# Performance work log

Hardware: AMD Instinct MI355X
Metric: run time of the kernel (lower is better)

Reference implementation:

```python
import jax, jax.numpy as jnp
import numpy as np

B, T, ENC, DEC, ATTN = 64, 2048, 512, 512, 256


def setup_inputs() -> dict:
    key = jax.random.key(0)
    k1, k2, k3, k4, k5, k6 = jax.random.split(key, 6)
    enc_out = jax.random.normal(k1, (B, T, ENC), dtype=jnp.float32)
    dec_hidden = jax.random.normal(k2, (B, DEC), dtype=jnp.float32)
    mask = jax.random.randint(k3, (B, T), 0, 2) == 1  # True = masked out
    # learned params (Linear with bias=False); torch Linear weight is [out,in],
    # we store transposed [in,out] for x @ W convention
    s_enc = 1.0 / np.sqrt(ENC)
    s_dec = 1.0 / np.sqrt(DEC)
    s_v = 1.0 / np.sqrt(ATTN)
    W_enc = jax.random.uniform(k4, (ENC, ATTN), jnp.float32, -s_enc, s_enc)
    W_dec = jax.random.uniform(k5, (DEC, ATTN), jnp.float32, -s_dec, s_dec)
    v = jax.random.uniform(k6, (ATTN,), jnp.float32, -s_v, s_v)
    return {"enc_out": enc_out, "dec_hidden": dec_hidden, "mask": mask,
            "W_enc": W_enc, "W_dec": W_dec, "v": v}


def reference(enc_out, dec_hidden, mask, W_enc, W_dec, v):
    # proj_enc: [B,T,A]; proj_dec: [B,1,A]
    proj_enc = jnp.einsum('bte,ea->bta', enc_out, W_enc)
    proj_dec = jnp.einsum('bd,da->ba', dec_hidden, W_dec)[:, None, :]
    # energy: [B,T] -- additive (Bahdanau) score
    energy = jnp.einsum('bta,a->bt', jnp.tanh(proj_enc + proj_dec), v)
    energy = jnp.where(mask, -jnp.inf, energy)
    attn_w = jax.nn.softmax(energy, axis=-1)
    attn_w = jnp.nan_to_num(attn_w, nan=0.0)  # fully-masked rows -> 0
    context = jnp.einsum('bt,bte->be', attn_w, enc_out)
    return context, attn_w
```

## Files before the change

### kernel.cpp

```cpp
#include <hip/hip_runtime.h>
#include <stdint.h>

#define Bx 64
#define Tx 2048
#define ENCx 512
#define ATTx 256

typedef float f4 __attribute__((ext_vector_type(4)));
typedef float f32x4 __attribute__((ext_vector_type(4)));
typedef short bf16x8 __attribute__((ext_vector_type(8)));

__device__ __forceinline__ unsigned short f2bf(float f) {
  union { float f; uint32_t u; } c; c.f = f;
  uint32_t u = c.u;
  u += 0x7fffu + ((u >> 16) & 1u);
  return (unsigned short)(u >> 16);
}

__device__ __forceinline__ uint32_t pk_bf(float lo, float hi) {
  uint32_t a = __float_as_uint(lo) + 0x8000u;
  uint32_t b = __float_as_uint(hi) + 0x8000u;
  return __builtin_amdgcn_perm(b, a, 0x07060302u);
}

__device__ __forceinline__ float ftanh(float x) {
  x = fminf(8.f, fmaxf(-8.f, x));
  float z = __expf(2.f * x);
  return 1.f - __fdividef(2.f, z + 1.f);
}

__global__ void k0_wt(const float* __restrict__ W, unsigned short* __restrict__ WTc) {
  int tid = blockIdx.x * 256 + threadIdx.x;
  int kc = tid >> 13;
  int r = tid & 8191;
  int n = r >> 5;
  int kk = r & 31;
  WTc[tid] = f2bf(W[(kc * 32 + kk) * ATTx + n]);
}

__global__ void k1_pd(const float* __restrict__ dec, const float* __restrict__ Wd,
                      float* __restrict__ pd) {
  __shared__ float ld[512];
  int b = blockIdx.x, a = threadIdx.x;
  ld[a] = dec[b * 512 + a];
  ld[a + 256] = dec[b * 512 + a + 256];
  __syncthreads();
  float s = 0.f;
#pragma unroll 8
  for (int d = 0; d < 512; ++d) s = fmaf(ld[d], Wd[d * ATTx + a], s);
  pd[b * ATTx + a] = s;
}

__global__ __launch_bounds__(256) void k2_energy(
    const float* __restrict__ enc, const unsigned short* __restrict__ WTc,
    const float* __restrict__ pd, const float* __restrict__ v,
    const int* __restrict__ mask, float* __restrict__ energy) {
  __shared__ float pdv[256];
  __shared__ float vvs[256];
  const int tid = threadIdx.x;
  const int wid = tid >> 6;
  const int lane = tid & 63;
  const int q = lane >> 4;
  const int c15 = lane & 15;
  const int m0 = blockIdx.x * 128;
  const int b = m0 >> 11;

  pdv[tid] = pd[b * ATTx + tid];
  vvs[tid] = v[tid];
  __syncthreads();

  const int mrow = m0 + wid * 32 + c15;
  const float* a0p = enc + (size_t)mrow * ENCx + q * 8;
  const float* a1p = a0p + 16 * ENCx;
  const unsigned short* wb = WTc + c15 * 32 + q * 8;

  f32x4 acc[2][16];
#pragma unroll
  for (int mt = 0; mt < 2; ++mt)
#pragma unroll
    for (int ct = 0; ct < 16; ++ct) { f32x4 z = {0.f,0.f,0.f,0.f}; acc[mt][ct] = z; }

  for (int kc = 0; kc < 16; ++kc) {
    f4 x0 = *(const f4*)(a0p + kc * 32);
    f4 x1 = *(const f4*)(a0p + kc * 32 + 4);
    f4 y0 = *(const f4*)(a1p + kc * 32);
    f4 y1 = *(const f4*)(a1p + kc * 32 + 4);
    bf16x8 bfr[16];
    const unsigned short* wkc = wb + kc * 8192;
#pragma unroll
    for (int ct = 0; ct < 16; ++ct)
      bfr[ct] = *(const bf16x8*)(wkc + ct * 512);

    union { uint32_t u[4]; bf16x8 v; } am0, am1;
    am0.u[0] = pk_bf(x0.x, x0.y); am0.u[1] = pk_bf(x0.z, x0.w);
    am0.u[2] = pk_bf(x1.x, x1.y); am0.u[3] = pk_bf(x1.z, x1.w);
    am1.u[0] = pk_bf(y0.x, y0.y); am1.u[1] = pk_bf(y0.z, y0.w);
    am1.u[2] = pk_bf(y1.x, y1.y); am1.u[3] = pk_bf(y1.z, y1.w);

#pragma unroll
    for (int ct = 0; ct < 16; ++ct) {
      acc[0][ct] = __builtin_amdgcn_mfma_f32_16x16x32_bf16(am0.v, bfr[ct], acc[0][ct], 0, 0, 0);
      acc[1][ct] = __builtin_amdgcn_mfma_f32_16x16x32_bf16(am1.v, bfr[ct], acc[1][ct], 0, 0, 0);
    }
  }

  float ps[2][4];
#pragma unroll
  for (int mt = 0; mt < 2; ++mt)
#pragma unroll
    for (int i = 0; i < 4; ++i) ps[mt][i] = 0.f;
#pragma unroll
  for (int ct = 0; ct < 16; ++ct) {
    float pv = pdv[ct * 16 + c15];
    float vv = vvs[ct * 16 + c15];
#pragma unroll
    for (int mt = 0; mt < 2; ++mt)
#pragma unroll
      for (int i = 0; i < 4; ++i)
        ps[mt][i] += ftanh(acc[mt][ct][i] + pv) * vv;
  }
#pragma unroll
  for (int s = 1; s < 16; s <<= 1)
#pragma unroll
    for (int mt = 0; mt < 2; ++mt)
#pragma unroll
      for (int i = 0; i < 4; ++i)
        ps[mt][i] += __shfl_xor(ps[mt][i], s, 64);
  if (c15 == 0) {
#pragma unroll
    for (int mt = 0; mt < 2; ++mt)
#pragma unroll
      for (int i = 0; i < 4; ++i) {
        int gm = m0 + wid * 32 + mt * 16 + q * 4 + i;
        energy[gm] = mask[gm] ? -1e30f : ps[mt][i];
      }
  }
}

__global__ void k3_softmax(const float* __restrict__ energy, float* __restrict__ attn) {
  __shared__ float redm[4];
  __shared__ float redl[4];
  int b = blockIdx.x, tid = threadIdx.x;
  int lane = tid & 63, wid = tid >> 6;
  float e[8];
#pragma unroll
  for (int i = 0; i < 8; ++i) e[i] = energy[b * Tx + tid + i * 256];
  float m = e[0];
#pragma unroll
  for (int i = 1; i < 8; ++i) m = fmaxf(m, e[i]);
#pragma unroll
  for (int s = 1; s < 64; s <<= 1) m = fmaxf(m, __shfl_xor(m, s, 64));
  if (lane == 0) redm[wid] = m;
  __syncthreads();
  m = fmaxf(fmaxf(redm[0], redm[1]), fmaxf(redm[2], redm[3]));
  bool dead = (m < -1e29f);
  float w[8];
  float l = 0.f;
#pragma unroll
  for (int i = 0; i < 8; ++i) { w[i] = dead ? 0.f : __expf(e[i] - m); l += w[i]; }
#pragma unroll
  for (int s = 1; s < 64; s <<= 1) l += __shfl_xor(l, s, 64);
  if (lane == 0) redl[wid] = l;
  __syncthreads();
  l = redl[0] + redl[1] + redl[2] + redl[3];
  float inv = dead ? 0.f : __fdividef(1.f, l);
#pragma unroll
  for (int i = 0; i < 8; ++i) attn[b * Tx + tid + i * 256] = w[i] * inv;
}

__global__ void k4_ctx(const float* __restrict__ enc, const float* __restrict__ attn,
                       float* __restrict__ part) {
  __shared__ float wl[128];
  __shared__ f4 comb[128];
  int tc = blockIdx.x & 15, b = blockIdx.x >> 4;
  int tid = threadIdx.x;
  if (tid < 128) wl[tid] = attn[b * Tx + tc * 128 + tid];
  __syncthreads();
  int tl = tid >> 7;
  int ef = tid & 127;
  f4 a = {0.f, 0.f, 0.f, 0.f};
  const f4* base = (const f4*)(enc + ((size_t)b * Tx + tc * 128) * ENCx) + ef;
  for (int t = tl; t < 128; t += 2) {
    f4 x = base[(size_t)t * 128];
    a += x * wl[t];
  }
  if (tl == 1) comb[ef] = a;
  __syncthreads();
  if (tl == 0) {
    a += comb[ef];
    *((f4*)(part + ((size_t)tc * 64 + b) * 512) + ef) = a;
  }
}

__global__ void k5_red(const float* __restrict__ part, float* __restrict__ ctx) {
  int idx = blockIdx.x * 256 + threadIdx.x;
  float s = 0.f;
#pragma unroll
  for (int tc = 0; tc < 16; ++tc) s += part[tc * 32768 + idx];
  ctx[idx] = s;
}

extern "C" void kernel_launch(void* const* d_in, const int* in_sizes, int n_in,
                              void* d_out, int out_size, void* d_ws, size_t ws_size,
                              hipStream_t stream) {
  const float* enc   = (const float*)d_in[0];
  const float* dec   = (const float*)d_in[1];
  const int*   mask  = (const int*)d_in[2];
  const float* W_enc = (const float*)d_in[3];
  const float* W_dec = (const float*)d_in[4];
  const float* v     = (const float*)d_in[5];
  float* ctx  = (float*)d_out;
  float* attn = ctx + Bx * ENCx;
  char* ws = (char*)d_ws;
  unsigned short* WTc = (unsigned short*)ws;
  float* pd     = (float*)(ws + 262144);
  float* energy = (float*)(ws + 262144 + 65536);
  float* part   = (float*)(ws + 262144 + 65536 + 524288);

  k0_wt<<<512, 256, 0, stream>>>(W_enc, WTc);
  k1_pd<<<64, 256, 0, stream>>>(dec, W_dec, pd);
  k2_energy<<<1024, 256, 0, stream>>>(enc, WTc, pd, v, mask, energy);
  k3_softmax<<<64, 256, 0, stream>>>(energy, attn);
  k4_ctx<<<1024, 256, 0, stream>>>(enc, attn, part);
  k5_red<<<128, 256, 0, stream>>>(part, ctx);
}
```

Baseline: 488.0 us.

## Split energy GEMM columns across waves and double the context grid

```diff
diff --git a/kernel.cpp b/kernel.cpp
--- a/kernel.cpp
+++ b/kernel.cpp
@@ -51,89 +51,105 @@
   pd[b * ATTx + a] = s;
 }
 
-__global__ __launch_bounds__(256) void k2_energy(
+__global__ __launch_bounds__(256, 4) void k2_energy(
     const float* __restrict__ enc, const unsigned short* __restrict__ WTc,
     const float* __restrict__ pd, const float* __restrict__ v,
     const int* __restrict__ mask, float* __restrict__ energy) {
   __shared__ float pdv[256];
   __shared__ float vvs[256];
+  __shared__ float ep[4][32];
   const int tid = threadIdx.x;
   const int wid = tid >> 6;
   const int lane = tid & 63;
   const int q = lane >> 4;
   const int c15 = lane & 15;
-  const int m0 = blockIdx.x * 128;
+  const int m0 = blockIdx.x * 32;
   const int b = m0 >> 11;
 
   pdv[tid] = pd[b * ATTx + tid];
   vvs[tid] = v[tid];
   __syncthreads();
 
-  const int mrow = m0 + wid * 32 + c15;
-  const float* a0p = enc + (size_t)mrow * ENCx + q * 8;
-  const float* a1p = a0p + 16 * ENCx;
-  const unsigned short* wb = WTc + c15 * 32 + q * 8;
-
-  f32x4 acc[2][16];
-#pragma unroll
-  for (int mt = 0; mt < 2; ++mt)
-#pragma unroll
-    for (int ct = 0; ct < 16; ++ct) { f32x4 z = {0.f,0.f,0.f,0.f}; acc[mt][ct] = z; }
-
+  const float* a0 = enc + (size_t)(m0 + c15) * ENCx + q * 8;
+  const float* a1 = a0 + 16 * ENCx;
+  const unsigned short* wb = WTc + (wid * 64 + c15) * 32 + q * 8;
+
+  f32x4 acc[2][4];
+#pragma unroll
+  for (int rt = 0; rt < 2; ++rt)
+#pragma unroll
+    for (int ct = 0; ct < 4; ++ct) { f32x4 z = {0.f,0.f,0.f,0.f}; acc[rt][ct] = z; }
+
+  f4 cur0a = *(const f4*)(a0);
+  f4 cur0b = *(const f4*)(a0 + 4);
+  f4 cur1a = *(const f4*)(a1);
+  f4 cur1b = *(const f4*)(a1 + 4);
+
+#pragma unroll 4
   for (int kc = 0; kc < 16; ++kc) {
-    f4 x0 = *(const f4*)(a0p + kc * 32);
-    f4 x1 = *(const f4*)(a0p + kc * 32 + 4);
-    f4 y0 = *(const f4*)(a1p + kc * 32);
-    f4 y1 = *(const f4*)(a1p + kc * 32 + 4);
-    bf16x8 bfr[16];
+    f4 nxt0a, nxt0b, nxt1a, nxt1b;
+    if (kc < 15) {
+      const float* p0 = a0 + (kc + 1) * 32;
+      const float* p1 = a1 + (kc + 1) * 32;
+      nxt0a = *(const f4*)(p0);
+      nxt0b = *(const f4*)(p0 + 4);
+      nxt1a = *(const f4*)(p1);
+      nxt1b = *(const f4*)(p1 + 4);
+    }
+    bf16x8 bfr[4];
     const unsigned short* wkc = wb + kc * 8192;
 #pragma unroll
-    for (int ct = 0; ct < 16; ++ct)
+    for (int ct = 0; ct < 4; ++ct)
       bfr[ct] = *(const bf16x8*)(wkc + ct * 512);
 
     union { uint32_t u[4]; bf16x8 v; } am0, am1;
-    am0.u[0] = pk_bf(x0.x, x0.y); am0.u[1] = pk_bf(x0.z, x0.w);
-    am0.u[2] = pk_bf(x1.x, x1.y); am0.u[3] = pk_bf(x1.z, x1.w);
-    am1.u[0] = pk_bf(y0.x, y0.y); am1.u[1] = pk_bf(y0.z, y0.w);
-    am1.u[2] = pk_bf(y1.x, y1.y); am1.u[3] = pk_bf(y1.z, y1.w);
-
-#pragma unroll
-    for (int ct = 0; ct < 16; ++ct) {
+    am0.u[0] = pk_bf(cur0a.x, cur0a.y); am0.u[1] = pk_bf(cur0a.z, cur0a.w);
+    am0.u[2] = pk_bf(cur0b.x, cur0b.y); am0.u[3] = pk_bf(cur0b.z, cur0b.w);
+    am1.u[0] = pk_bf(cur1a.x, cur1a.y); am1.u[1] = pk_bf(cur1a.z, cur1a.w);
+    am1.u[2] = pk_bf(cur1b.x, cur1b.y); am1.u[3] = pk_bf(cur1b.z, cur1b.w);
+
+#pragma unroll
+    for (int ct = 0; ct < 4; ++ct) {
       acc[0][ct] = __builtin_amdgcn_mfma_f32_16x16x32_bf16(am0.v, bfr[ct], acc[0][ct], 0, 0, 0);
       acc[1][ct] = __builtin_amdgcn_mfma_f32_16x16x32_bf16(am1.v, bfr[ct], acc[1][ct], 0, 0, 0);
     }
+    cur0a = nxt0a; cur0b = nxt0b; cur1a = nxt1a; cur1b = nxt1b;
   }
 
   float ps[2][4];
 #pragma unroll
-  for (int mt = 0; mt < 2; ++mt)
-#pragma unroll
-    for (int i = 0; i < 4; ++i) ps[mt][i] = 0.f;
-#pragma unroll
-  for (int ct = 0; ct < 16; ++ct) {
-    float pv = pdv[ct * 16 + c15];
-    float vv = vvs[ct * 16 + c15];
-#pragma unroll
-    for (int mt = 0; mt < 2; ++mt)
+  for (int rt = 0; rt < 2; ++rt)
+#pragma unroll
+    for (int i = 0; i < 4; ++i) ps[rt][i] = 0.f;
+#pragma unroll
+  for (int ct = 0; ct < 4; ++ct) {
+    int col = wid * 64 + ct * 16 + c15;
+    float pv = pdv[col];
+    float vv = vvs[col];
+#pragma unroll
+    for (int rt = 0; rt < 2; ++rt)
 #pragma unroll
       for (int i = 0; i < 4; ++i)
-        ps[mt][i] += ftanh(acc[mt][ct][i] + pv) * vv;
+        ps[rt][i] += ftanh(acc[rt][ct][i] + pv) * vv;
   }
 #pragma unroll
   for (int s = 1; s < 16; s <<= 1)
 #pragma unroll
-    for (int mt = 0; mt < 2; ++mt)
+    for (int rt = 0; rt < 2; ++rt)
 #pragma unroll
       for (int i = 0; i < 4; ++i)
-        ps[mt][i] += __shfl_xor(ps[mt][i], s, 64);
-  if (c15 == 0) {
-#pragma unroll
-    for (int mt = 0; mt < 2; ++mt)
-#pragma unroll
-      for (int i = 0; i < 4; ++i) {
-        int gm = m0 + wid * 32 + mt * 16 + q * 4 + i;
-        energy[gm] = mask[gm] ? -1e30f : ps[mt][i];
-      }
+        ps[rt][i] += __shfl_xor(ps[rt][i], s, 64);
+  if (c15 == 0)
+#pragma unroll
+    for (int rt = 0; rt < 2; ++rt)
+#pragma unroll
+      for (int i = 0; i < 4; ++i)
+        ep[wid][rt * 16 + q * 4 + i] = ps[rt][i];
+  __syncthreads();
+  if (tid < 32) {
+    float e = ep[0][tid] + ep[1][tid] + ep[2][tid] + ep[3][tid];
+    int gm = m0 + tid;
+    energy[gm] = mask[gm] ? -1e30f : e;
   }
 }
 
@@ -168,25 +184,30 @@
   for (int i = 0; i < 8; ++i) attn[b * Tx + tid + i * 256] = w[i] * inv;
 }
 
-__global__ void k4_ctx(const float* __restrict__ enc, const float* __restrict__ attn,
-                       float* __restrict__ part) {
-  __shared__ float wl[128];
+__global__ __launch_bounds__(256) void k4_ctx(const float* __restrict__ enc,
+                                              const float* __restrict__ attn,
+                                              float* __restrict__ part) {
+  __shared__ float wl[64];
   __shared__ f4 comb[128];
-  int tc = blockIdx.x & 15, b = blockIdx.x >> 4;
+  int tc = blockIdx.x & 31, b = blockIdx.x >> 5;
   int tid = threadIdx.x;
-  if (tid < 128) wl[tid] = attn[b * Tx + tc * 128 + tid];
-  __syncthreads();
-  int tl = tid >> 7;
+  if (tid < 64) wl[tid] = attn[b * Tx + tc * 64 + tid];
+  __syncthreads();
+  int tg = tid >> 7;
   int ef = tid & 127;
+  const f4* base = (const f4*)(enc + ((size_t)b * Tx + tc * 64 + tg * 32) * ENCx) + ef;
   f4 a = {0.f, 0.f, 0.f, 0.f};
-  const f4* base = (const f4*)(enc + ((size_t)b * Tx + tc * 128) * ENCx) + ef;
-  for (int t = tl; t < 128; t += 2) {
-    f4 x = base[(size_t)t * 128];
-    a += x * wl[t];
-  }
-  if (tl == 1) comb[ef] = a;
-  __syncthreads();
-  if (tl == 0) {
+#pragma unroll
+  for (int j0 = 0; j0 < 32; j0 += 8) {
+    f4 x[8];
+#pragma unroll
+    for (int u = 0; u < 8; ++u) x[u] = base[(size_t)(j0 + u) * 128];
+#pragma unroll
+    for (int u = 0; u < 8; ++u) a += x[u] * wl[tg * 32 + j0 + u];
+  }
+  if (tg == 1) comb[ef] = a;
+  __syncthreads();
+  if (tg == 0) {
     a += comb[ef];
     *((f4*)(part + ((size_t)tc * 64 + b) * 512) + ef) = a;
   }
@@ -196,7 +217,7 @@
   int idx = blockIdx.x * 256 + threadIdx.x;
   float s = 0.f;
 #pragma unroll
-  for (int tc = 0; tc < 16; ++tc) s += part[tc * 32768 + idx];
+  for (int tc = 0; tc < 32; ++tc) s += part[tc * 32768 + idx];
   ctx[idx] = s;
 }
 
@@ -219,8 +240,8 @@
 
   k0_wt<<<512, 256, 0, stream>>>(W_enc, WTc);
   k1_pd<<<64, 256, 0, stream>>>(dec, W_dec, pd);
-  k2_energy<<<1024, 256, 0, stream>>>(enc, WTc, pd, v, mask, energy);
+  k2_energy<<<4096, 256, 0, stream>>>(enc, WTc, pd, v, mask, energy);
   k3_softmax<<<64, 256, 0, stream>>>(energy, attn);
-  k4_ctx<<<1024, 256, 0, stream>>>(enc, attn, part);
+  k4_ctx<<<2048, 256, 0, stream>>>(enc, attn, part);
   k5_red<<<128, 256, 0, stream>>>(part, ctx);
 }
```

Result: slower. 544.4 us (+11.6%).
